# Kernel tuning notes

Measured on AMD Instinct MI355X. Metric: run time of the kernel, lower is better.

The kernel has to match this reference:

```python
import jax, jax.numpy as jnp
import numpy as np

E, TOPK, H, I, NSH = 8, 2, 2048, 5120, 2
B, S = 2, 1024


def setup_inputs() -> dict:
    key = jax.random.key(0)
    ks = jax.random.split(key, 8)
    sc = 0.02
    return {
        "x": jax.random.normal(ks[0], (B, S, H), dtype=jnp.float32),
        "w_router": jax.random.normal(ks[1], (E, H), dtype=jnp.float32),
        "wg": jax.random.normal(ks[2], (E, I, H), dtype=jnp.float32) * sc,
        "wu": jax.random.normal(ks[3], (E, I, H), dtype=jnp.float32) * sc,
        "wd": jax.random.normal(ks[4], (E, H, I), dtype=jnp.float32) * sc,
        "sg": jax.random.normal(ks[5], (NSH, I, H), dtype=jnp.float32) * sc,
        "su": jax.random.normal(ks[6], (NSH, I, H), dtype=jnp.float32) * sc,
        "sd": jax.random.normal(ks[7], (NSH, H, I), dtype=jnp.float32) * sc,
    }


def reference(x, w_router, wg, wu, wd, sg, su, sd):
    b, s, h = x.shape
    xt = x.reshape(-1, h)  # [T, H]
    T = xt.shape[0]

    # Router: fp32 linear, sigmoid scores, top-k, renormalize
    logits = jnp.einsum('th,eh->te', xt.astype(jnp.float32), w_router.astype(jnp.float32))
    scores = jax.nn.sigmoid(logits)
    topk_w, topk_i = jax.lax.top_k(scores, TOPK)
    topk_w = topk_w / jnp.sum(topk_w, axis=-1, keepdims=True)

    # Dense combine weights [T, E]: zero for non-selected experts
    comb = jnp.zeros((T, E), dtype=xt.dtype)
    comb = comb.at[jnp.arange(T)[:, None], topk_i].add(topk_w.astype(xt.dtype))

    # Routed experts (SwiGLU, no bias): compute all, combine with sparse weights
    gate = jax.nn.silu(jnp.einsum('th,eih->tei', xt, wg))
    up = jnp.einsum('th,eih->tei', xt, wu)
    expert_out = jnp.einsum('tei,ehi->teh', gate * up, wd)
    out = jnp.einsum('te,teh->th', comb, expert_out)

    # Shared experts: applied to every token, summed
    sgate = jax.nn.silu(jnp.einsum('th,jih->tji', xt, sg))
    sup = jnp.einsum('th,jih->tji', xt, su)
    out = out + jnp.einsum('tji,jhi->th', sgate * sup, sd)

    return out.reshape(b, s, h)
```

## Files before the change

### kernel.cpp

```cpp
#include <hip/hip_runtime.h>
#include <stdint.h>


#define E_ 8
#define H_ 2048
#define I_ 5120
#define T_ 2048
#define NSLOT 10

typedef __attribute__((ext_vector_type(4))) float f32x4;
typedef __attribute__((ext_vector_type(8))) __bf16 bf16x8;
typedef __attribute__((ext_vector_type(4))) unsigned int u32x4;
typedef __attribute__((ext_vector_type(2))) unsigned int u32x2;

__device__ __forceinline__ int sw(int r) { return (r ^ (r >> 2)) & 3; }

__device__ __forceinline__ unsigned short f2bf(float f) {
  unsigned u = __builtin_bit_cast(unsigned, f);
  u += 0x7FFFu + ((u >> 16) & 1u);
  return (unsigned short)(u >> 16);
}

__device__ __forceinline__ u32x2 cvt4(f32x4 v) {
  unsigned r0, r1;
  asm("v_cvt_pk_bf16_f32 %0, %1, %2" : "=v"(r0) : "v"(v[0]), "v"(v[1]));
  asm("v_cvt_pk_bf16_f32 %0, %1, %2" : "=v"(r1) : "v"(v[2]), "v"(v[3]));
  u32x2 w; w[0] = r0; w[1] = r1;
  return w;
}

__global__ __launch_bounds__(256) void k_castx(const float* __restrict__ x,
                                               unsigned short* __restrict__ xb) {
  const int i = (blockIdx.x * 256 + threadIdx.x) * 8;
  f32x4 a = *(const f32x4*)(x + i);
  f32x4 b = *(const f32x4*)(x + i + 4);
  u32x2 lo = cvt4(a), hi = cvt4(b);
  u32x4 o; o[0] = lo[0]; o[1] = lo[1]; o[2] = hi[0]; o[3] = hi[1];
  *(u32x4*)(xb + i) = o;
}

__global__ __launch_bounds__(64) void k_router(const float* __restrict__ x,
                                               const float* __restrict__ wr,
                                               int* __restrict__ tki,
                                               float* __restrict__ tkw) {
  const int t = blockIdx.x, lane = threadIdx.x;
  const float* xr = x + (size_t)t * H_;
  float lg[E_];
#pragma unroll
  for (int e = 0; e < E_; ++e) {
    const float* w = wr + (size_t)e * H_;
    float acc = 0.f;
    for (int k = lane; k < H_; k += 64) acc += xr[k] * w[k];
#pragma unroll
    for (int off = 32; off > 0; off >>= 1) acc += __shfl_down(acc, off);
    lg[e] = acc;
  }
  if (lane == 0) {
    float sc[E_];
#pragma unroll
    for (int e = 0; e < E_; ++e) sc[e] = 1.f / (1.f + expf(-lg[e]));
    int b0 = 0;
#pragma unroll
    for (int e = 1; e < E_; ++e) if (sc[e] > sc[b0]) b0 = e;
    int b1 = -1;
#pragma unroll
    for (int e = 0; e < E_; ++e) {
      if (e == b0) continue;
      if (b1 < 0 || sc[e] > sc[b1]) b1 = e;
    }
    float s0 = sc[b0], s1 = sc[b1], inv = 1.f / (s0 + s1);
    tki[2 * t] = b0; tki[2 * t + 1] = b1;
    tkw[2 * t] = s0 * inv; tkw[2 * t + 1] = s1 * inv;
  }
}

__global__ __launch_bounds__(64) void k_lists(const int* __restrict__ tki,
                                              const float* __restrict__ tkw,
                                              int* __restrict__ elist,
                                              float* __restrict__ ew,
                                              int* __restrict__ ecnt) {
  const int s = blockIdx.x, lane = threadIdx.x;
  if (s < E_) {
    int base = 0;
    for (int c = 0; c < T_ / 64; ++c) {
      int t = c * 64 + lane;
      int i0 = tki[2 * t], i1 = tki[2 * t + 1];
      int flag = (i0 == s) ? 1 : ((i1 == s) ? 2 : 0);
      unsigned long long m = __ballot(flag != 0);
      int pre = __popcll(m & ((1ull << lane) - 1ull));
      if (flag) {
        elist[s * T_ + base + pre] = t;
        ew[s * T_ + base + pre] = tkw[2 * t + flag - 1];
      }
      base += __popcll(m);
    }
    int padded = (base + 255) & ~255;
    for (int p = base + lane; p < padded; p += 64) { elist[s * T_ + p] = 0; ew[s * T_ + p] = 0.f; }
    if (lane == 0) ecnt[s] = base;
  } else {
    for (int i = lane; i < T_; i += 64) { elist[s * T_ + i] = i; ew[s * T_ + i] = 1.f; }
    if (lane == 0) ecnt[s] = T_;
  }
}

__global__ void k_bases(const int* __restrict__ ecnt, int* __restrict__ sbase) {
  if (threadIdx.x == 0 && blockIdx.x == 0) {
    int b = 0;
    for (int s = 0; s < NSLOT; ++s) { sbase[s] = b; b += (ecnt[s] + 255) & ~255; }
  }
}

__global__ __launch_bounds__(1024, 4) void k_gateup(
    const unsigned short* __restrict__ xb,
    const float* __restrict__ wg_all, const float* __restrict__ wu_all,
    const float* __restrict__ sg_all, const float* __restrict__ su_all,
    const int* __restrict__ elist, const float* __restrict__ ew,
    const int* __restrict__ ecnt,
    const int* __restrict__ sbase, unsigned short* __restrict__ h) {
  const int s = blockIdx.z;
  const int cnt = ecnt[s];
  const int r0 = blockIdx.y * 256;
  if (r0 >= cnt) return;
  const int n0 = blockIdx.x * 128;
  const float* gw; const float* uw;
  if (s < E_) { gw = wg_all + (size_t)s * I_ * H_; uw = wu_all + (size_t)s * I_ * H_; }
  else        { gw = sg_all + (size_t)(s - E_) * I_ * H_; uw = su_all + (size_t)(s - E_) * I_ * H_; }
  const int* lst = elist + s * T_;
  const int hrow0 = sbase[s] + r0;

  __shared__ u32x4 sA[2][256 * 4];
  __shared__ u32x4 sG[2][128 * 4];
  __shared__ u32x4 sU[2][128 * 4];

  const int tid = threadIdx.x;
  const int w = tid >> 6, lane = tid & 63;
  const int wr = w >> 2, wc = w & 3;
  const int fr = lane & 15, k8 = lane >> 4;

  const int ar = tid >> 2, ca = tid & 3;
  int li = r0 + ar; if (li >= cnt) li = r0;
  const unsigned short* xp = xb + (size_t)lst[li] * H_ + ca * 8;
  const int br = tid >> 3, cb = (tid & 7) >> 1, bh = tid & 1;
  const float* gp = gw + (size_t)(n0 + br) * H_ + (tid & 7) * 4;
  const float* up = uw + (size_t)(n0 + br) * H_ + (tid & 7) * 4;

  u32x4 ra; f32x4 rg, ru;

  f32x4 accg[4][2], accu[4][2];
#pragma unroll
  for (int m = 0; m < 4; ++m)
#pragma unroll
    for (int n = 0; n < 2; ++n) {
      accg[m][n] = (f32x4){0.f, 0.f, 0.f, 0.f};
      accu[m][n] = (f32x4){0.f, 0.f, 0.f, 0.f};
    }

  auto loadNext = [&]() {
    ra = *(const u32x4*)xp; rg = *(const f32x4*)gp; ru = *(const f32x4*)up;
    xp += 32; gp += 32; up += 32;
  };
  auto stage = [&](int b) {
    sA[b][ar * 4 + (ca ^ sw(ar))] = ra;
    ((u32x2*)&sG[b][br * 4 + (cb ^ sw(br))])[bh] = cvt4(rg);
    ((u32x2*)&sU[b][br * 4 + (cb ^ sw(br))])[bh] = cvt4(ru);
  };
  auto compute = [&](int b) {
    bf16x8 af[4], gf[2], uf[2];
#pragma unroll
    for (int m = 0; m < 4; ++m) {
      int r = wr * 64 + m * 16 + fr;
      af[m] = __builtin_bit_cast(bf16x8, sA[b][r * 4 + (k8 ^ sw(r))]);
    }
#pragma unroll
    for (int n = 0; n < 2; ++n) {
      int r = wc * 32 + n * 16 + fr;
      gf[n] = __builtin_bit_cast(bf16x8, sG[b][r * 4 + (k8 ^ sw(r))]);
      uf[n] = __builtin_bit_cast(bf16x8, sU[b][r * 4 + (k8 ^ sw(r))]);
    }
#pragma unroll
    for (int m = 0; m < 4; ++m)
#pragma unroll
      for (int n = 0; n < 2; ++n) {
        accg[m][n] = __builtin_amdgcn_mfma_f32_16x16x32_bf16(af[m], gf[n], accg[m][n], 0, 0, 0);
        accu[m][n] = __builtin_amdgcn_mfma_f32_16x16x32_bf16(af[m], uf[n], accu[m][n], 0, 0, 0);
      }
  };

  const int KT = H_ / 32;
  loadNext();
  stage(0);
  loadNext();
  __syncthreads();
  int cur = 0;
  for (int kt = 0; kt < KT; ++kt) {
    compute(cur);
    if (kt + 1 < KT) {
      stage(cur ^ 1);
      if (kt + 2 < KT) loadNext();
      __syncthreads();
      cur ^= 1;
    }
  }

#pragma unroll
  for (int m = 0; m < 4; ++m)
#pragma unroll
    for (int r = 0; r < 4; ++r) {
      int rit = wr * 64 + m * 16 + k8 * 4 + r;
      if (r0 + rit < cnt) {
        float wgt = ew[s * T_ + r0 + rit];
        unsigned short* hrow = h + (size_t)(hrow0 + rit) * I_ + n0 + wc * 32;
#pragma unroll
        for (int n = 0; n < 2; ++n) {
          float g = accg[m][n][r], uv = accu[m][n][r];
          float hv = g / (1.f + expf(-g)) * uv * wgt;
          hrow[n * 16 + fr] = f2bf(hv);
        }
      }
    }
}

__global__ __launch_bounds__(1024, 4) void k_down(
    const unsigned short* __restrict__ h,
    const float* __restrict__ wd_all, const float* __restrict__ sd_all,
    const int* __restrict__ elist,
    const int* __restrict__ ecnt, const int* __restrict__ sbase,
    float* __restrict__ out) {
  const int s = blockIdx.z;
  const int cnt = ecnt[s];
  const int r0 = blockIdx.y * 256;
  if (r0 >= cnt) return;
  const int n0 = blockIdx.x * 256;
  const float* bw = (s < E_) ? wd_all + (size_t)s * H_ * I_
                             : sd_all + (size_t)(s - E_) * H_ * I_;
  const int hrow0 = sbase[s] + r0;

  __shared__ u32x4 sA[2][256 * 4];
  __shared__ u32x4 sB[2][256 * 4];

  const int tid = threadIdx.x;
  const int w = tid >> 6, lane = tid & 63;
  const int wr = w >> 2, wc = w & 3;
  const int fr = lane & 15, k8 = lane >> 4;

  const int ar = tid >> 2, ca = tid & 3;
  const unsigned short* hp = h + (size_t)(hrow0 + ar) * I_ + ca * 8;
  const int brr = tid >> 2, cbD = tid & 3;
  const float* bp = bw + (size_t)(n0 + brr) * I_ + cbD * 8;

  u32x4 ra; f32x4 rb0, rb1;

  f32x4 acc[4][4];
#pragma unroll
  for (int m = 0; m < 4; ++m)
#pragma unroll
    for (int n = 0; n < 4; ++n) acc[m][n] = (f32x4){0.f, 0.f, 0.f, 0.f};

  auto loadNext = [&]() {
    ra = *(const u32x4*)hp; hp += 32;
    rb0 = *(const f32x4*)bp; rb1 = *(const f32x4*)(bp + 4); bp += 32;
  };
  auto stage = [&](int b) {
    sA[b][ar * 4 + (ca ^ sw(ar))] = ra;
    u32x2 lo = cvt4(rb0), hi = cvt4(rb1);
    u32x4 q; q[0] = lo[0]; q[1] = lo[1]; q[2] = hi[0]; q[3] = hi[1];
    sB[b][brr * 4 + (cbD ^ sw(brr))] = q;
  };
  auto compute = [&](int b) {
    bf16x8 af[4], bf[4];
#pragma unroll
    for (int m = 0; m < 4; ++m) {
      int r = wr * 64 + m * 16 + fr;
      af[m] = __builtin_bit_cast(bf16x8, sA[b][r * 4 + (k8 ^ sw(r))]);
    }
#pragma unroll
    for (int n = 0; n < 4; ++n) {
      int r = wc * 64 + n * 16 + fr;
      bf[n] = __builtin_bit_cast(bf16x8, sB[b][r * 4 + (k8 ^ sw(r))]);
    }
#pragma unroll
    for (int m = 0; m < 4; ++m)
#pragma unroll
      for (int n = 0; n < 4; ++n)
        acc[m][n] = __builtin_amdgcn_mfma_f32_16x16x32_bf16(af[m], bf[n], acc[m][n], 0, 0, 0);
  };

  const int KT = I_ / 32;
  loadNext();
  stage(0);
  loadNext();
  __syncthreads();
  int cur = 0;
  for (int kt = 0; kt < KT; ++kt) {
    compute(cur);
    if (kt + 1 < KT) {
      stage(cur ^ 1);
      if (kt + 2 < KT) loadNext();
      __syncthreads();
      cur ^= 1;
    }
  }

  const int* lst = elist + s * T_;
#pragma unroll
  for (int m = 0; m < 4; ++m)
#pragma unroll
    for (int r = 0; r < 4; ++r) {
      int rit = wr * 64 + m * 16 + k8 * 4 + r;
      if (r0 + rit < cnt) {
        int t = lst[r0 + rit];
        float* orow = out + (size_t)t * H_ + n0 + wc * 64 + fr;
#pragma unroll
        for (int n = 0; n < 4; ++n) atomicAdd(orow + n * 16, acc[m][n][r]);
      }
    }
}

extern "C" void kernel_launch(void* const* d_in, const int* in_sizes, int n_in,
                              void* d_out, int out_size, void* d_ws, size_t ws_size,
                              hipStream_t stream) {
  const float* x  = (const float*)d_in[0];
  const float* wr = (const float*)d_in[1];
  const float* wg = (const float*)d_in[2];
  const float* wu = (const float*)d_in[3];
  const float* wd = (const float*)d_in[4];
  const float* sg = (const float*)d_in[5];
  const float* su = (const float*)d_in[6];
  const float* sd = (const float*)d_in[7];
  float* out = (float*)d_out;
  char* ws = (char*)d_ws;

  int*   tki   = (int*)(ws);
  float* tkw   = (float*)(ws + 16384);
  int*   elist = (int*)(ws + 32768);
  float* ew    = (float*)(ws + 114688);
  int*   ecnt  = (int*)(ws + 196608);
  int*   sbase = (int*)(ws + 196864);
  unsigned short* xb = (unsigned short*)(ws + 262144);
  unsigned short* h  = (unsigned short*)(ws + 262144 + 8388608);

  k_castx<<<T_ * H_ / (256 * 8), 256, 0, stream>>>(x, xb);
  k_router<<<T_, 64, 0, stream>>>(x, wr, tki, tkw);
  k_lists<<<NSLOT, 64, 0, stream>>>(tki, tkw, elist, ew, ecnt);
  k_bases<<<1, 1, 0, stream>>>(ecnt, sbase);
  k_gateup<<<dim3(I_ / 128, T_ / 256, NSLOT), 1024, 0, stream>>>(
      xb, wg, wu, sg, su, elist, ew, ecnt, sbase, h);
  hipMemsetAsync(out, 0, (size_t)T_ * H_ * sizeof(float), stream);
  k_down<<<dim3(H_ / 256, T_ / 256, NSLOT), 1024, 0, stream>>>(
      h, wd, sd, elist, ecnt, sbase, out);
}
```

Before: 978.9 us.

## Use direct global-to-LDS DMA loads with triple buffering in expert GEMMs

Replaces the register-staged global loads in the gate/up and down GEMM kernels with global_load_lds direct-to-LDS copies into a three-stage ring buffer, synchronised by explicit vmcnt waits and barriers. Weights are now stored in LDS as fp32 and converted to bf16 at fragment-read time, with a new XOR swizzle for the wider rows. This removes per-thread staging registers and store instructions and deepens prefetch to overlap memory with MFMA, but triples and doubles LDS footprint, which may reduce occupancy, and adds conversion work inside the inner loop.

```diff
diff --git a/kernel.cpp b/kernel.cpp
--- a/kernel.cpp
+++ b/kernel.cpp
@@ -14,6 +14,12 @@
 typedef __attribute__((ext_vector_type(2))) unsigned int u32x2;
 
 __device__ __forceinline__ int sw(int r) { return (r ^ (r >> 2)) & 3; }
+
+typedef __attribute__((address_space(1))) const void* gptr1_t;
+typedef __attribute__((address_space(3))) void* lptr3_t;
+__device__ __forceinline__ void load_lds16(const void* g, void* l) {
+  __builtin_amdgcn_global_load_lds((gptr1_t)g, (lptr3_t)l, 16, 0, 0);
+}
 
 __device__ __forceinline__ unsigned short f2bf(float f) {
   unsigned u = __builtin_bit_cast(unsigned, f);
@@ -28,6 +34,21 @@
   u32x2 w; w[0] = r0; w[1] = r1;
   return w;
 }
+
+__device__ __forceinline__ bf16x8 cvt8(u32x4 a, u32x4 b) {
+  f32x4 fa = __builtin_bit_cast(f32x4, a), fb = __builtin_bit_cast(f32x4, b);
+  u32x2 lo = cvt4(fa), hi = cvt4(fb);
+  u32x4 q; q[0] = lo[0]; q[1] = lo[1]; q[2] = hi[0]; q[3] = hi[1];
+  return __builtin_bit_cast(bf16x8, q);
+}
+
+#define PIPE_SYNC(N)                                        \
+  do {                                                      \
+    asm volatile("s_waitcnt vmcnt(" #N ")" ::: "memory");   \
+    __builtin_amdgcn_sched_barrier(0);                      \
+    __builtin_amdgcn_s_barrier();                           \
+    __builtin_amdgcn_sched_barrier(0);                      \
+  } while (0)
 
 __global__ __launch_bounds__(256) void k_castx(const float* __restrict__ x,
                                                unsigned short* __restrict__ xb) {
@@ -128,23 +149,29 @@
   const int* lst = elist + s * T_;
   const int hrow0 = sbase[s] + r0;
 
-  __shared__ u32x4 sA[2][256 * 4];
-  __shared__ u32x4 sG[2][128 * 4];
-  __shared__ u32x4 sU[2][128 * 4];
+  __shared__ u32x4 sA[3][1024];
+  __shared__ u32x4 sG[3][1024];
+  __shared__ u32x4 sU[3][1024];
 
   const int tid = threadIdx.x;
-  const int w = tid >> 6, lane = tid & 63;
-  const int wr = w >> 2, wc = w & 3;
+  const int wv = tid >> 6, lane = tid & 63;
+  const int wr = wv >> 2, wc = wv & 3;
   const int fr = lane & 15, k8 = lane >> 4;
 
-  const int ar = tid >> 2, ca = tid & 3;
-  int li = r0 + ar; if (li >= cnt) li = r0;
-  const unsigned short* xp = xb + (size_t)lst[li] * H_ + ca * 8;
-  const int br = tid >> 3, cb = (tid & 7) >> 1, bh = tid & 1;
-  const float* gp = gw + (size_t)(n0 + br) * H_ + (tid & 7) * 4;
-  const float* up = uw + (size_t)(n0 + br) * H_ + (tid & 7) * 4;
-
-  u32x4 ra; f32x4 rg, ru;
+  const int arow = wv * 16 + (lane >> 2);
+  int li = r0 + arow; if (li >= cnt) li = r0;
+  const unsigned short* aSrc =
+      xb + (size_t)lst[li] * H_ + (((lane & 3) ^ sw(arow)) * 8);
+  const int grow = wv * 8 + (lane >> 3);
+  const int gco = ((lane & 7) ^ (grow & 7)) * 4;
+  const float* gSrc = gw + (size_t)(n0 + grow) * H_ + gco;
+  const float* uSrc = uw + (size_t)(n0 + grow) * H_ + gco;
+
+  auto dma = [&](int b, int kt) {
+    load_lds16(aSrc + kt * 32, &sA[b][wv * 64]);
+    load_lds16(gSrc + kt * 32, &sG[b][wv * 64]);
+    load_lds16(uSrc + kt * 32, &sU[b][wv * 64]);
+  };
 
   f32x4 accg[4][2], accu[4][2];
 #pragma unroll
@@ -155,15 +182,6 @@
       accu[m][n] = (f32x4){0.f, 0.f, 0.f, 0.f};
     }
 
-  auto loadNext = [&]() {
-    ra = *(const u32x4*)xp; rg = *(const f32x4*)gp; ru = *(const f32x4*)up;
-    xp += 32; gp += 32; up += 32;
-  };
-  auto stage = [&](int b) {
-    sA[b][ar * 4 + (ca ^ sw(ar))] = ra;
-    ((u32x2*)&sG[b][br * 4 + (cb ^ sw(br))])[bh] = cvt4(rg);
-    ((u32x2*)&sU[b][br * 4 + (cb ^ sw(br))])[bh] = cvt4(ru);
-  };
   auto compute = [&](int b) {
     bf16x8 af[4], gf[2], uf[2];
 #pragma unroll
@@ -174,8 +192,13 @@
 #pragma unroll
     for (int n = 0; n < 2; ++n) {
       int r = wc * 32 + n * 16 + fr;
-      gf[n] = __builtin_bit_cast(bf16x8, sG[b][r * 4 + (k8 ^ sw(r))]);
-      uf[n] = __builtin_bit_cast(bf16x8, sU[b][r * 4 + (k8 ^ sw(r))]);
+      int s8 = r & 7;
+      u32x4 g0 = sG[b][r * 8 + ((2 * k8) ^ s8)];
+      u32x4 g1 = sG[b][r * 8 + ((2 * k8 + 1) ^ s8)];
+      u32x4 u0 = sU[b][r * 8 + ((2 * k8) ^ s8)];
+      u32x4 u1 = sU[b][r * 8 + ((2 * k8 + 1) ^ s8)];
+      gf[n] = cvt8(g0, g1);
+      uf[n] = cvt8(u0, u1);
     }
 #pragma unroll
     for (int m = 0; m < 4; ++m)
@@ -187,19 +210,18 @@
   };
 
   const int KT = H_ / 32;
-  loadNext();
-  stage(0);
-  loadNext();
-  __syncthreads();
+  dma(0, 0); dma(1, 1);
+  PIPE_SYNC(3);
   int cur = 0;
   for (int kt = 0; kt < KT; ++kt) {
+    int nx = cur + 2; if (nx >= 3) nx -= 3;
+    if (kt + 2 < KT) dma(nx, kt + 2);
     compute(cur);
     if (kt + 1 < KT) {
-      stage(cur ^ 1);
-      if (kt + 2 < KT) loadNext();
-      __syncthreads();
-      cur ^= 1;
-    }
+      if (kt + 2 < KT) PIPE_SYNC(3);
+      else             PIPE_SYNC(0);
+    }
+    cur = (cur == 2) ? 0 : cur + 1;
   }
 
 #pragma unroll
@@ -235,20 +257,27 @@
                              : sd_all + (size_t)(s - E_) * H_ * I_;
   const int hrow0 = sbase[s] + r0;
 
-  __shared__ u32x4 sA[2][256 * 4];
-  __shared__ u32x4 sB[2][256 * 4];
+  __shared__ u32x4 sA[3][1024];
+  __shared__ u32x4 sB[3][2048];
 
   const int tid = threadIdx.x;
-  const int w = tid >> 6, lane = tid & 63;
-  const int wr = w >> 2, wc = w & 3;
+  const int wv = tid >> 6, lane = tid & 63;
+  const int wr = wv >> 2, wc = wv & 3;
   const int fr = lane & 15, k8 = lane >> 4;
 
-  const int ar = tid >> 2, ca = tid & 3;
-  const unsigned short* hp = h + (size_t)(hrow0 + ar) * I_ + ca * 8;
-  const int brr = tid >> 2, cbD = tid & 3;
-  const float* bp = bw + (size_t)(n0 + brr) * I_ + cbD * 8;
-
-  u32x4 ra; f32x4 rb0, rb1;
+  const int arow = wv * 16 + (lane >> 2);
+  const unsigned short* aSrc =
+      h + (size_t)(hrow0 + arow) * I_ + (((lane & 3) ^ sw(arow)) * 8);
+  const int brow0 = wv * 16 + (lane >> 3);
+  const int brow1 = brow0 + 8;
+  const float* bSrc0 = bw + (size_t)(n0 + brow0) * I_ + ((lane & 7) ^ (brow0 & 7)) * 4;
+  const float* bSrc1 = bw + (size_t)(n0 + brow1) * I_ + ((lane & 7) ^ (brow1 & 7)) * 4;
+
+  auto dma = [&](int b, int kt) {
+    load_lds16(aSrc + kt * 32, &sA[b][wv * 64]);
+    load_lds16(bSrc0 + kt * 32, &sB[b][wv * 128]);
+    load_lds16(bSrc1 + kt * 32, &sB[b][wv * 128 + 64]);
+  };
 
   f32x4 acc[4][4];
 #pragma unroll
@@ -256,16 +285,6 @@
 #pragma unroll
     for (int n = 0; n < 4; ++n) acc[m][n] = (f32x4){0.f, 0.f, 0.f, 0.f};
 
-  auto loadNext = [&]() {
-    ra = *(const u32x4*)hp; hp += 32;
-    rb0 = *(const f32x4*)bp; rb1 = *(const f32x4*)(bp + 4); bp += 32;
-  };
-  auto stage = [&](int b) {
-    sA[b][ar * 4 + (ca ^ sw(ar))] = ra;
-    u32x2 lo = cvt4(rb0), hi = cvt4(rb1);
-    u32x4 q; q[0] = lo[0]; q[1] = lo[1]; q[2] = hi[0]; q[3] = hi[1];
-    sB[b][brr * 4 + (cbD ^ sw(brr))] = q;
-  };
   auto compute = [&](int b) {
     bf16x8 af[4], bf[4];
 #pragma unroll
@@ -276,7 +295,10 @@
 #pragma unroll
     for (int n = 0; n < 4; ++n) {
       int r = wc * 64 + n * 16 + fr;
-      bf[n] = __builtin_bit_cast(bf16x8, sB[b][r * 4 + (k8 ^ sw(r))]);
+      int s8 = r & 7;
+      u32x4 b0 = sB[b][r * 8 + ((2 * k8) ^ s8)];
+      u32x4 b1 = sB[b][r * 8 + ((2 * k8 + 1) ^ s8)];
+      bf[n] = cvt8(b0, b1);
     }
 #pragma unroll
     for (int m = 0; m < 4; ++m)
@@ -286,19 +308,18 @@
   };
 
   const int KT = I_ / 32;
-  loadNext();
-  stage(0);
-  loadNext();
-  __syncthreads();
+  dma(0, 0); dma(1, 1);
+  PIPE_SYNC(3);
   int cur = 0;
   for (int kt = 0; kt < KT; ++kt) {
+    int nx = cur + 2; if (nx >= 3) nx -= 3;
+    if (kt + 2 < KT) dma(nx, kt + 2);
     compute(cur);
     if (kt + 1 < KT) {
-      stage(cur ^ 1);
-      if (kt + 2 < KT) loadNext();
-      __syncthreads();
-      cur ^= 1;
-    }
+      if (kt + 2 < KT) PIPE_SYNC(3);
+      else             PIPE_SYNC(0);
+    }
+    cur = (cur == 2) ? 0 : cur + 1;
   }
 
   const int* lst = elist + s * T_;
```

Result: slower. 1.396 ms (+42.6%).

## Split-K the down projection and shrink its tile to raise block count

Applied to the files above, without the earlier changes.

The down-projection kernel now splits the I reduction into four chunks across blocks and uses 256x128 output tiles with 512 threads instead of 256x256 with 1024. This multiplies the number of blocks so more CUs have work for the small routed-expert token counts. The cost is that each weight tile is reloaded by more row blocks, and the output accumulation relies on atomics or adds into the zeroed output across k-splits (epilogue not shown).

```diff
diff --git a/kernel.cpp b/kernel.cpp
--- a/kernel.cpp
+++ b/kernel.cpp
@@ -220,7 +220,8 @@
     }
 }
 
-__global__ __launch_bounds__(1024, 4) void k_down(
+#define KSPLIT 4
+__global__ __launch_bounds__(512, 4) void k_down(
     const unsigned short* __restrict__ h,
     const float* __restrict__ wd_all, const float* __restrict__ sd_all,
     const int* __restrict__ elist,
@@ -230,25 +231,28 @@
   const int cnt = ecnt[s];
   const int r0 = blockIdx.y * 256;
   if (r0 >= cnt) return;
-  const int n0 = blockIdx.x * 256;
+  const int nt = blockIdx.x & 15;
+  const int ks = blockIdx.x >> 4;
+  const int n0 = nt * 128;
+  const int kbase = ks * (I_ / KSPLIT);
   const float* bw = (s < E_) ? wd_all + (size_t)s * H_ * I_
                              : sd_all + (size_t)(s - E_) * H_ * I_;
   const int hrow0 = sbase[s] + r0;
 
   __shared__ u32x4 sA[2][256 * 4];
-  __shared__ u32x4 sB[2][256 * 4];
+  __shared__ u32x4 sB[2][128 * 4];
 
   const int tid = threadIdx.x;
-  const int w = tid >> 6, lane = tid & 63;
-  const int wr = w >> 2, wc = w & 3;
+  const int wv = tid >> 6, lane = tid & 63;
+  const int wr = wv >> 1, wc = wv & 1;
   const int fr = lane & 15, k8 = lane >> 4;
 
-  const int ar = tid >> 2, ca = tid & 3;
-  const unsigned short* hp = h + (size_t)(hrow0 + ar) * I_ + ca * 8;
-  const int brr = tid >> 2, cbD = tid & 3;
-  const float* bp = bw + (size_t)(n0 + brr) * I_ + cbD * 8;
-
-  u32x4 ra; f32x4 rb0, rb1;
+  const int ar = tid >> 1, ca2 = (tid & 1) * 2;
+  const unsigned short* hp = h + (size_t)(hrow0 + ar) * I_ + kbase + ca2 * 8;
+  const int brr = tid >> 2, cb = tid & 3;
+  const float* bp = bw + (size_t)(n0 + brr) * I_ + kbase + cb * 8;
+
+  u32x4 ra0, ra1; f32x4 rb0, rb1;
 
   f32x4 acc[4][4];
 #pragma unroll
@@ -257,14 +261,15 @@
     for (int n = 0; n < 4; ++n) acc[m][n] = (f32x4){0.f, 0.f, 0.f, 0.f};
 
   auto loadNext = [&]() {
-    ra = *(const u32x4*)hp; hp += 32;
+    ra0 = *(const u32x4*)hp; ra1 = *(const u32x4*)(hp + 8); hp += 32;
     rb0 = *(const f32x4*)bp; rb1 = *(const f32x4*)(bp + 4); bp += 32;
   };
   auto stage = [&](int b) {
-    sA[b][ar * 4 + (ca ^ sw(ar))] = ra;
+    sA[b][ar * 4 + (ca2 ^ sw(ar))] = ra0;
+    sA[b][ar * 4 + ((ca2 + 1) ^ sw(ar))] = ra1;
     u32x2 lo = cvt4(rb0), hi = cvt4(rb1);
     u32x4 q; q[0] = lo[0]; q[1] = lo[1]; q[2] = hi[0]; q[3] = hi[1];
-    sB[b][brr * 4 + (cbD ^ sw(brr))] = q;
+    sB[b][brr * 4 + (cb ^ sw(brr))] = q;
   };
   auto compute = [&](int b) {
     bf16x8 af[4], bf[4];
@@ -285,7 +290,7 @@
         acc[m][n] = __builtin_amdgcn_mfma_f32_16x16x32_bf16(af[m], bf[n], acc[m][n], 0, 0, 0);
   };
 
-  const int KT = I_ / 32;
+  const int KT = I_ / 32 / KSPLIT;
   loadNext();
   stage(0);
   loadNext();
@@ -346,6 +351,6 @@
   k_gateup<<<dim3(I_ / 128, T_ / 256, NSLOT), 1024, 0, stream>>>(
       xb, wg, wu, sg, su, elist, ew, ecnt, sbase, h);
   hipMemsetAsync(out, 0, (size_t)T_ * H_ * sizeof(float), stream);
-  k_down<<<dim3(H_ / 256, T_ / 256, NSLOT), 1024, 0, stream>>>(
+  k_down<<<dim3((H_ / 128) * KSPLIT, T_ / 256, NSLOT), 512, 0, stream>>>(
       h, wd, sd, elist, ecnt, sbase, out);
 }
```

Result: slower. 1.0000 ms (+2.1%).
